# Performance work log

Hardware: AMD Instinct MI355X
Metric: run time of the kernel (lower is better)

The kernel has to match this reference:

```python
import jax, jax.numpy as jnp
import numpy as np

B, C, INF, H, W = 4, 64, 64, 64, 64
DQK = INF // 8  # query/key channels (inf_dim // 8)


def setup_inputs() -> dict:
    key = jax.random.key(0)
    ks = jax.random.split(key, 9)
    s = 0.05
    return {
        "x": jax.random.normal(ks[0], (B, C, H, W), dtype=jnp.float32),
        "inf": jax.random.normal(ks[1], (B, INF, H, W), dtype=jnp.float32),
        "Wq": jax.random.normal(ks[2], (DQK, INF), dtype=jnp.float32) * s,
        "bq": jax.random.normal(ks[3], (DQK,), dtype=jnp.float32) * s,
        "Wk": jax.random.normal(ks[4], (DQK, INF), dtype=jnp.float32) * s,
        "bk": jax.random.normal(ks[5], (DQK,), dtype=jnp.float32) * s,
        "Wv": jax.random.normal(ks[6], (C, C), dtype=jnp.float32) * s,
        "bv": jax.random.normal(ks[7], (C,), dtype=jnp.float32) * s,
        "gamma": jax.random.normal(ks[8], (1,), dtype=jnp.float32),
    }


def reference(x, inf, Wq, bq, Wk, bk, Wv, bv, gamma):
    b, c, h, w = x.shape
    n = h * w
    # 1x1 convs == per-pixel channel matmuls
    q = jnp.einsum("oc,bchw->bohw", Wq, inf) + bq[None, :, None, None]  # [B,DQK,H,W]
    k = jnp.einsum("oc,bchw->bohw", Wk, inf) + bk[None, :, None, None]  # [B,DQK,H,W]
    v = jnp.einsum("oc,bchw->bohw", Wv, x) + bv[None, :, None, None]    # [B,C,H,W]
    q = q.reshape(b, -1, n)  # [B,DQK,N]
    k = k.reshape(b, -1, n)  # [B,DQK,N]
    v = v.reshape(b, c, n)   # [B,C,N]
    # energy[b,i,j] = q_i . k_j  (unscaled)
    energy = jnp.einsum("bdi,bdj->bij", q, k)  # [B,N,N]
    attention = jax.nn.softmax(energy, axis=-1)
    # out[b,c,m] = sum_n v[b,c,n] * attention[b,m,n]
    out = jnp.einsum("bcn,bmn->bcm", v, attention)
    out = out.reshape(b, c, h, w)
    return gamma[0] * out + x
```

## Files before the change

kernel.cpp:

```cpp
#include <hip/hip_runtime.h>
#include <hip/hip_bf16.h>
#include <stdint.h>


typedef float    f32x16 __attribute__((ext_vector_type(16)));
typedef short    bf16x8 __attribute__((ext_vector_type(8)));
typedef unsigned int   u32;
typedef unsigned short u16;
typedef u32 u32x4 __attribute__((ext_vector_type(4)));

#define LOG2E 1.4426950408889634f

__device__ __forceinline__ u32 bfr(float f){
  u32 u = __float_as_uint(f);
  return (u + 0x7FFFu + ((u >> 16) & 1u)) >> 16;
}
__device__ __forceinline__ u32 pk2(float lo, float hi){
  return bfr(lo) | (bfr(hi) << 16);
}
__device__ __forceinline__ bf16x8 mk_frag(u32 a, u32 b, u32 c, u32 d){
  union { u32 u[4]; bf16x8 v; } t; t.u[0]=a; t.u[1]=b; t.u[2]=c; t.u[3]=d; return t.v;
}
__device__ __forceinline__ bf16x8 pack8(float t0,float t1,float t2,float t3,
                                        float t4,float t5,float t6,float t7){
  return mk_frag(pk2(t0,t1), pk2(t2,t3), pk2(t4,t5), pk2(t6,t7));
}
__device__ __forceinline__ f32x16 mfma32(bf16x8 a, bf16x8 b, f32x16 c){
  return __builtin_amdgcn_mfma_f32_32x32x16_bf16(a, b, c, 0, 0, 0);
}
__device__ __forceinline__ bf16x8 lds_frag(const char* p){
  union { u32x4 u; bf16x8 f; } t; t.u = *(const u32x4*)p; return t.f;
}
#if __has_builtin(__builtin_amdgcn_exp2f)
#define EXP2(x) __builtin_amdgcn_exp2f(x)
#else
#define EXP2(x) exp2f(x)
#endif
__device__ __forceinline__ float sclamp(float s){
  return fminf(fmaxf(s, -80.f), 80.f);
}

__global__ __launch_bounds__(128, 1) void qkv_k(
    const float* __restrict__ x, const float* __restrict__ inf,
    const float* __restrict__ Wq, const float* __restrict__ bq,
    const float* __restrict__ Wk, const float* __restrict__ bk,
    const float* __restrict__ Wv, const float* __restrict__ bv,
    u32* __restrict__ qp, u32* __restrict__ kp, u16* __restrict__ vb)
{
  __shared__ float bias[80];
  const int tid = threadIdx.x;
  if (tid < 64)      bias[tid] = bv[tid];
  else if (tid < 72) bias[tid] = bq[tid-64]*LOG2E;
  else if (tid < 80) bias[tid] = bk[tid-72];
  __syncthreads();
  const int w = tid >> 6, lane = tid & 63, ln = lane & 31, hi = lane >> 5;
  const int b  = blockIdx.x >> 6;
  const int n0 = (blockIdx.x & 63)*64 + w*32;
  const int n  = n0 + ln;

  bf16x8 wvf[2][4];
#pragma unroll
  for (int mt = 0; mt < 2; ++mt)
#pragma unroll
    for (int ks = 0; ks < 4; ++ks){
      const float* s = Wv + (mt*32+ln)*64 + ks*16 + hi*8;
      wvf[mt][ks] = pack8(s[0],s[1],s[2],s[3],s[4],s[5],s[6],s[7]);
    }
  bf16x8 w2f[4];
#pragma unroll
  for (int ks = 0; ks < 4; ++ks){
    float t[8];
#pragma unroll
    for (int i = 0; i < 8; ++i){
      float v = 0.f;
      if (ln < 8)       v = Wq[ln*64 + ks*16 + hi*8 + i]*LOG2E;
      else if (ln < 16) v = Wk[(ln-8)*64 + ks*16 + hi*8 + i];
      t[i] = v;
    }
    w2f[ks] = pack8(t[0],t[1],t[2],t[3],t[4],t[5],t[6],t[7]);
  }

  f32x16 dqk = {}; f32x16 dv0 = {}; f32x16 dv1 = {};
#pragma unroll
  for (int ks = 0; ks < 4; ++ks){
    const float* ip = inf + (size_t)(b*64 + ks*16 + hi*8)*4096 + n;
    bf16x8 bi = pack8(ip[0], ip[4096], ip[2*4096], ip[3*4096],
                      ip[4*4096], ip[5*4096], ip[6*4096], ip[7*4096]);
    dqk = mfma32(w2f[ks], bi, dqk);
    const float* xp = x + (size_t)(b*64 + ks*16 + hi*8)*4096 + n;
    bf16x8 bx = pack8(xp[0], xp[4096], xp[2*4096], xp[3*4096],
                      xp[4*4096], xp[5*4096], xp[6*4096], xp[7*4096]);
    dv0 = mfma32(wvf[0][ks], bx, dv0);
    dv1 = mfma32(wvf[1][ks], bx, dv1);
  }
  {
    u32 q0 = pk2(dqk[0]+bias[64+4*hi+0], dqk[1]+bias[64+4*hi+1]);
    u32 q1 = pk2(dqk[2]+bias[64+4*hi+2], dqk[3]+bias[64+4*hi+3]);
    u32 k0 = pk2(dqk[4]+bias[72+4*hi+0], dqk[5]+bias[72+4*hi+1]);
    u32 k1 = pk2(dqk[6]+bias[72+4*hi+2], dqk[7]+bias[72+4*hi+3]);
    u32* qd = qp + (size_t)(b*4096 + n)*8 + hi*2;
    qd[0] = q0; qd[1] = q1; qd[4] = 0u; qd[5] = 0u;
    u32* kd = kp + (size_t)(b*4096 + n)*8 + hi*2;
    kd[0] = k0; kd[1] = k1; kd[4] = 0u; kd[5] = 0u;
  }
#pragma unroll
  for (int mt = 0; mt < 2; ++mt){
    const f32x16 dv = mt ? dv1 : dv0;
#pragma unroll
    for (int r = 0; r < 16; ++r){
      const int c = mt*32 + (r&3) + 8*(r>>2) + 4*hi;
      vb[(size_t)(b*64 + c)*4096 + n] = (u16)bfr(dv[r] + bias[c]);
    }
  }
}

__global__ __launch_bounds__(256, 2) void attn_k(
    const u32* __restrict__ qp, const u32* __restrict__ kp, const u16* __restrict__ vb,
    const float* __restrict__ x, const float* __restrict__ gamma,
    float* __restrict__ out)
{
  __shared__ __align__(16) char smem[40960];
  const int tid = threadIdx.x, w = tid >> 6, lane = tid & 63, ln = lane & 31, hi = lane >> 5;
  const int b = blockIdx.x >> 7, mt = blockIdx.x & 127;
  const int m0 = mt * 32;
  char* const base = smem + w*10240;

  const bf16x8 qf = *(const bf16x8*)(qp + (size_t)(b*4096 + m0 + ln)*8 + hi*4);

  const char* kptr = (const char*)kp + (size_t)(b*4096 + w*1024)*32 + lane*32;
  const char* vptr = (const char*)vb + ((size_t)(b*64 + (lane>>3))*4096 + w*1024)*2
                     + (lane&7)*16;
  const int vds = (lane>>3)*128 + (((lane&7)*16) ^ ((lane>>3)<<4));

  u32x4 kst0, kst1, vst0, vst1, vst2, vst3, vst4, vst5, vst6, vst7;
#define LOADJ                                                 \
  kst0 = *(const u32x4*)(kptr); kst1 = *(const u32x4*)(kptr+16); \
  vst0 = *(const u32x4*)(vptr);           vst1 = *(const u32x4*)(vptr+65536);   \
  vst2 = *(const u32x4*)(vptr+2*65536);   vst3 = *(const u32x4*)(vptr+3*65536); \
  vst4 = *(const u32x4*)(vptr+4*65536);   vst5 = *(const u32x4*)(vptr+5*65536); \
  vst6 = *(const u32x4*)(vptr+6*65536);   vst7 = *(const u32x4*)(vptr+7*65536)
#define WRITEJ                                                 \
  *(u32x4*)(base + lane*32) = kst0; *(u32x4*)(base + lane*32 + 16) = kst1;     \
  { char* vB_ = base + 2048 + vds;                                             \
    *(u32x4*)(vB_)        = vst0; *(u32x4*)(vB_ + 1024) = vst1;                \
    *(u32x4*)(vB_ + 2048) = vst2; *(u32x4*)(vB_ + 3072) = vst3;                \
    *(u32x4*)(vB_ + 4096) = vst4; *(u32x4*)(vB_ + 5120) = vst5;                \
    *(u32x4*)(vB_ + 6144) = vst6; *(u32x4*)(vB_ + 7168) = vst7; }

  LOADJ;

  f32x16 acc0 = {}; f32x16 acc1 = {};
  float rs = 0.f;

  for (int j = 0; j < 16; ++j){
    WRITEJ;
    if (j < 15){ kptr += 2048; vptr += 128; LOADJ; }
    __syncthreads();

    const bf16x8 ka0 = lds_frag(base + ln*32 + hi*16);
    const bf16x8 ka1 = lds_frag(base + 1024 + ln*32 + hi*16);
    const f32x16 z = {};
    const f32x16 st0 = mfma32(ka0, qf, z);
    const f32x16 st1 = mfma32(ka1, qf, z);

    float p0[16], p1[16];
#pragma unroll
    for (int r = 0; r < 16; ++r) p0[r] = EXP2(sclamp(st0[r]));
#pragma unroll
    for (int r = 0; r < 16; ++r) p1[r] = EXP2(sclamp(st1[r]));
    float t0 = 0.f, t1 = 0.f;
#pragma unroll
    for (int r = 0; r < 16; ++r){ t0 += p0[r]; t1 += p1[r]; }
    rs += t0 + t1;

    bf16x8 b2[4];
#pragma unroll
    for (int g = 0; g < 4; ++g){
      const float* pp = (g & 2) ? p1 : p0;
      const int o = (g & 1) * 8;
      u32 x0 = pk2(pp[o+0], pp[o+1]), x1 = pk2(pp[o+2], pp[o+3]);
      u32 x2 = pk2(pp[o+4], pp[o+5]), x3 = pk2(pp[o+6], pp[o+7]);
      u32 s0 = __shfl_xor(x0, 32), s1 = __shfl_xor(x1, 32);
      u32 s2 = __shfl_xor(x2, 32), s3 = __shfl_xor(x3, 32);
      b2[g] = mk_frag(hi ? s2 : x0, hi ? s3 : x1,
                      hi ? x2 : s0, hi ? x3 : s1);
    }

    const char* vB = base + 2048;
    const int sw = (ln & 7) << 4;
#pragma unroll
    for (int ks = 0; ks < 4; ++ks){
      const bf16x8 vf0 = lds_frag(vB + ln*128 + ((ks*32 + hi*16) ^ sw));
      acc0 = mfma32(vf0, b2[ks], acc0);
      const bf16x8 vf1 = lds_frag(vB + (32+ln)*128 + ((ks*32 + hi*16) ^ sw));
      acc1 = mfma32(vf1, b2[ks], acc1);
    }
    __syncthreads();
  }
#undef LOADJ
#undef WRITEJ

  const float rt = rs + __shfl_xor(rs, 32);

  float* accS = (float*)base;
#pragma unroll
  for (int r = 0; r < 16; ++r){
    const int c = (r&3) + 8*(r>>2) + 4*hi;
    accS[c*32 + ln]      = acc0[r];
    accS[(32+c)*32 + ln] = acc1[r];
  }
  if (lane < 32) ((float*)(base + 8192))[ln] = rt;
  __syncthreads();

  const float g = gamma[0];
  float rtot = 0.f;
#pragma unroll
  for (int ww = 0; ww < 4; ++ww)
    rtot += ((const float*)(smem + ww*10240 + 8192))[ln];
  const float rinv = g / rtot;
#pragma unroll
  for (int i = 0; i < 8; ++i){
    const int c = w*16 + hi*8 + i;
    float s = 0.f;
#pragma unroll
    for (int ww = 0; ww < 4; ++ww)
      s += ((const float*)(smem + ww*10240))[c*32 + ln];
    const size_t o = (size_t)(b*64 + c)*4096 + m0 + ln;
    out[o] = s * rinv + x[o];
  }
}

extern "C" void kernel_launch(void* const* d_in, const int* in_sizes, int n_in,
                              void* d_out, int out_size, void* d_ws, size_t ws_size,
                              hipStream_t stream)
{
  (void)in_sizes; (void)n_in; (void)out_size; (void)ws_size;
  const float* x   = (const float*)d_in[0];
  const float* inf = (const float*)d_in[1];
  const float* Wq  = (const float*)d_in[2];
  const float* bq  = (const float*)d_in[3];
  const float* Wk  = (const float*)d_in[4];
  const float* bk  = (const float*)d_in[5];
  const float* Wv  = (const float*)d_in[6];
  const float* bv  = (const float*)d_in[7];
  const float* gm  = (const float*)d_in[8];
  float* out = (float*)d_out;

  char* ws = (char*)d_ws;
  u32* qp = (u32*)(ws);
  u32* kp = (u32*)(ws + 524288);
  u16* vb = (u16*)(ws + 1048576);

  qkv_k<<<dim3(256), dim3(128), 0, stream>>>(x, inf, Wq, bq, Wk, bk, Wv, bv, qp, kp, vb);
  attn_k<<<dim3(512), dim3(256), 0, stream>>>(qp, kp, vb, x, gm, out);
}
```

Before: 118.1 us.

## Split key range across eight waves and load K fragments directly from global

The attention block grows from 4 to 8 waves, so each wave walks half as many key chunks (8 instead of 16) and the cross-wave reduction now sums 8 partial accumulators. K fragments are read straight from global memory into registers and prefetched one step ahead, rather than staged through LDS. This is meant to add latency hiding and cut LDS traffic, at the cost of a larger shared buffer (64KB), more reduction work and extra barriers, and a higher launch-bounds occupancy request.

```diff
diff --git a/kernel.cpp b/kernel.cpp
--- a/kernel.cpp
+++ b/kernel.cpp
@@ -28,7 +28,7 @@
 __device__ __forceinline__ f32x16 mfma32(bf16x8 a, bf16x8 b, f32x16 c){
   return __builtin_amdgcn_mfma_f32_32x32x16_bf16(a, b, c, 0, 0, 0);
 }
-__device__ __forceinline__ bf16x8 lds_frag(const char* p){
+__device__ __forceinline__ bf16x8 frag16(const char* p){
   union { u32x4 u; bf16x8 f; } t; t.u = *(const u32x4*)p; return t.f;
 }
 #if __has_builtin(__builtin_amdgcn_exp2f)
@@ -114,54 +114,53 @@
   }
 }
 
-__global__ __launch_bounds__(256, 2) void attn_k(
+__global__ __launch_bounds__(512, 4) void attn_k(
     const u32* __restrict__ qp, const u32* __restrict__ kp, const u16* __restrict__ vb,
     const float* __restrict__ x, const float* __restrict__ gamma,
     float* __restrict__ out)
 {
-  __shared__ __align__(16) char smem[40960];
+  __shared__ __align__(16) char smem[65536];
   const int tid = threadIdx.x, w = tid >> 6, lane = tid & 63, ln = lane & 31, hi = lane >> 5;
   const int b = blockIdx.x >> 7, mt = blockIdx.x & 127;
   const int m0 = mt * 32;
-  char* const base = smem + w*10240;
+  char* const base = smem + w*8192;
 
   const bf16x8 qf = *(const bf16x8*)(qp + (size_t)(b*4096 + m0 + ln)*8 + hi*4);
 
-  const char* kptr = (const char*)kp + (size_t)(b*4096 + w*1024)*32 + lane*32;
-  const char* vptr = (const char*)vb + ((size_t)(b*64 + (lane>>3))*4096 + w*1024)*2
+  const char* vptr = (const char*)vb + ((size_t)(b*64 + (lane>>3))*4096 + w*512)*2
                      + (lane&7)*16;
   const int vds = (lane>>3)*128 + (((lane&7)*16) ^ ((lane>>3)<<4));
-
-  u32x4 kst0, kst1, vst0, vst1, vst2, vst3, vst4, vst5, vst6, vst7;
-#define LOADJ                                                 \
-  kst0 = *(const u32x4*)(kptr); kst1 = *(const u32x4*)(kptr+16); \
+  const char* kb = (const char*)kp + (size_t)(b*4096 + w*512)*32 + ln*32 + hi*16;
+
+  u32x4 vst0, vst1, vst2, vst3, vst4, vst5, vst6, vst7;
+#define LOADV                                                 \
   vst0 = *(const u32x4*)(vptr);           vst1 = *(const u32x4*)(vptr+65536);   \
   vst2 = *(const u32x4*)(vptr+2*65536);   vst3 = *(const u32x4*)(vptr+3*65536); \
   vst4 = *(const u32x4*)(vptr+4*65536);   vst5 = *(const u32x4*)(vptr+5*65536); \
   vst6 = *(const u32x4*)(vptr+6*65536);   vst7 = *(const u32x4*)(vptr+7*65536)
-#define WRITEJ                                                 \
-  *(u32x4*)(base + lane*32) = kst0; *(u32x4*)(base + lane*32 + 16) = kst1;     \
-  { char* vB_ = base + 2048 + vds;                                             \
+#define WRITEV                                                 \
+  { char* vB_ = base + vds;                                                    \
     *(u32x4*)(vB_)        = vst0; *(u32x4*)(vB_ + 1024) = vst1;                \
     *(u32x4*)(vB_ + 2048) = vst2; *(u32x4*)(vB_ + 3072) = vst3;                \
     *(u32x4*)(vB_ + 4096) = vst4; *(u32x4*)(vB_ + 5120) = vst5;                \
     *(u32x4*)(vB_ + 6144) = vst6; *(u32x4*)(vB_ + 7168) = vst7; }
 
-  LOADJ;
+  LOADV;
+  bf16x8 ka0 = frag16(kb);
+  bf16x8 ka1 = frag16(kb + 1024);
 
   f32x16 acc0 = {}; f32x16 acc1 = {};
   float rs = 0.f;
 
-  for (int j = 0; j < 16; ++j){
-    WRITEJ;
-    if (j < 15){ kptr += 2048; vptr += 128; LOADJ; }
+  for (int j = 0; j < 8; ++j){
+    WRITEV;
+    if (j < 7){ vptr += 128; LOADV; }
     __syncthreads();
 
-    const bf16x8 ka0 = lds_frag(base + ln*32 + hi*16);
-    const bf16x8 ka1 = lds_frag(base + 1024 + ln*32 + hi*16);
     const f32x16 z = {};
     const f32x16 st0 = mfma32(ka0, qf, z);
     const f32x16 st1 = mfma32(ka1, qf, z);
+    if (j < 7){ kb += 2048; ka0 = frag16(kb); ka1 = frag16(kb + 1024); }
 
     float p0[16], p1[16];
 #pragma unroll
@@ -186,21 +185,30 @@
                       hi ? x2 : s0, hi ? x3 : s1);
     }
 
-    const char* vB = base + 2048;
     const int sw = (ln & 7) << 4;
 #pragma unroll
     for (int ks = 0; ks < 4; ++ks){
-      const bf16x8 vf0 = lds_frag(vB + ln*128 + ((ks*32 + hi*16) ^ sw));
+      const bf16x8 vf0 = frag16(base + ln*128 + ((ks*32 + hi*16) ^ sw));
       acc0 = mfma32(vf0, b2[ks], acc0);
-      const bf16x8 vf1 = lds_frag(vB + (32+ln)*128 + ((ks*32 + hi*16) ^ sw));
+      const bf16x8 vf1 = frag16(base + (32+ln)*128 + ((ks*32 + hi*16) ^ sw));
       acc1 = mfma32(vf1, b2[ks], acc1);
     }
     __syncthreads();
   }
-#undef LOADJ
-#undef WRITEJ
+#undef LOADV
+#undef WRITEV
 
   const float rt = rs + __shfl_xor(rs, 32);
+
+  __syncthreads();
+  if (lane < 32) ((float*)smem)[w*32 + ln] = rt;
+  __syncthreads();
+  float rtot = 0.f;
+#pragma unroll
+  for (int ww = 0; ww < 8; ++ww)
+    rtot += ((const float*)smem)[ww*32 + ln];
+  const float rinv = gamma[0] / rtot;
+  __syncthreads();
 
   float* accS = (float*)base;
 #pragma unroll
@@ -209,22 +217,15 @@
     accS[c*32 + ln]      = acc0[r];
     accS[(32+c)*32 + ln] = acc1[r];
   }
-  if (lane < 32) ((float*)(base + 8192))[ln] = rt;
-  __syncthreads();
-
-  const float g = gamma[0];
-  float rtot = 0.f;
-#pragma unroll
-  for (int ww = 0; ww < 4; ++ww)
-    rtot += ((const float*)(smem + ww*10240 + 8192))[ln];
-  const float rinv = g / rtot;
-#pragma unroll
-  for (int i = 0; i < 8; ++i){
-    const int c = w*16 + hi*8 + i;
+  __syncthreads();
+
+#pragma unroll
+  for (int i = 0; i < 4; ++i){
+    const int c = w*8 + hi*4 + i;
     float s = 0.f;
 #pragma unroll
-    for (int ww = 0; ww < 4; ++ww)
-      s += ((const float*)(smem + ww*10240))[c*32 + ln];
+    for (int ww = 0; ww < 8; ++ww)
+      s += ((const float*)(smem + ww*8192))[c*32 + ln];
     const size_t o = (size_t)(b*64 + c)*4096 + m0 + ln;
     out[o] = s * rinv + x[o];
   }
@@ -252,5 +253,5 @@
   u16* vb = (u16*)(ws + 1048576);
 
   qkv_k<<<dim3(256), dim3(128), 0, stream>>>(x, inf, Wq, bq, Wk, bk, Wv, bv, qp, kp, vb);
-  attn_k<<<dim3(512), dim3(256), 0, stream>>>(qp, kp, vb, x, gm, out);
-}
+  attn_k<<<dim3(512), dim3(512), 0, stream>>>(qp, kp, vb, x, gm, out);
+}
```

After: 113.0 us. 4.3% less time.
